# Kernel tuning notes

Hardware: AMD Instinct MI355X
Metric: run time of the kernel (lower is better)

The kernel has to match this reference:

```python
import jax, jax.numpy as jnp
import numpy as np

D = 64          # node_hidden_dim
MP_STEPS = 6    # num_step_message_passing
S2S_STEPS = 6   # num_step_set2set
LSTM_LAYERS = 3 # num_layer_set2set


def setup_inputs() -> dict:
    key = jax.random.key(0)
    ks = jax.random.split(key, 32)
    N, E, B = 10000, 50000, 500
    node_in, edge_in, edge_hid, out_dim = 15, 5, 128, 12
    s = 0.1
    inp = {}
    inp["node_feat"] = jax.random.normal(ks[0], (N, node_in), jnp.float32)
    inp["edge_feat"] = jax.random.normal(ks[1], (E, edge_in), jnp.float32)
    inp["src"] = jax.random.randint(ks[2], (E,), 0, N)
    inp["dst"] = jax.random.randint(ks[3], (E,), 0, N)
    inp["graph_ids"] = jnp.sort(jax.random.randint(ks[4], (N,), 0, B))
    inp["num_graphs"] = B
    # lin0
    inp["lin0_W"] = jax.random.normal(ks[5], (node_in, D), jnp.float32) * s
    inp["lin0_b"] = jnp.zeros((D,), jnp.float32)
    # edge network MLP (Linear -> ReLU -> Linear), output reshaped to D x D per edge
    inp["em_W1"] = jax.random.normal(ks[6], (edge_in, edge_hid), jnp.float32) * s
    inp["em_b1"] = jnp.zeros((edge_hid,), jnp.float32)
    inp["em_W2"] = jax.random.normal(ks[7], (edge_hid, D * D), jnp.float32) * 0.02
    inp["em_b2"] = jnp.zeros((D * D,), jnp.float32)
    inp["conv_bias"] = jnp.zeros((D,), jnp.float32)
    # GRU (input D, hidden D), torch layout: [3*D, in], gate order r,z,n
    inp["gru_Wih"] = jax.random.normal(ks[8], (3 * D, D), jnp.float32) * s
    inp["gru_Whh"] = jax.random.normal(ks[9], (3 * D, D), jnp.float32) * s
    inp["gru_bih"] = jnp.zeros((3 * D,), jnp.float32)
    inp["gru_bhh"] = jnp.zeros((3 * D,), jnp.float32)
    # Set2Set LSTM: input 2*D, hidden D, 3 layers. torch layout [4*D, in], gates i,f,g,o
    inp["lstm0_Wih"] = jax.random.normal(ks[10], (4 * D, 2 * D), jnp.float32) * s
    inp["lstm0_Whh"] = jax.random.normal(ks[11], (4 * D, D), jnp.float32) * s
    inp["lstm0_bih"] = jnp.zeros((4 * D,), jnp.float32)
    inp["lstm0_bhh"] = jnp.zeros((4 * D,), jnp.float32)
    inp["lstm12_Wih"] = jax.random.normal(ks[12], (2, 4 * D, D), jnp.float32) * s
    inp["lstm12_Whh"] = jax.random.normal(ks[13], (2, 4 * D, D), jnp.float32) * s
    inp["lstm12_bih"] = jnp.zeros((2, 4 * D), jnp.float32)
    inp["lstm12_bhh"] = jnp.zeros((2, 4 * D), jnp.float32)
    # output head
    inp["lin1_W"] = jax.random.normal(ks[14], (2 * D, D), jnp.float32) * s
    inp["lin1_b"] = jnp.zeros((D,), jnp.float32)
    inp["lin2_W"] = jax.random.normal(ks[15], (D, out_dim), jnp.float32) * s
    inp["lin2_b"] = jnp.zeros((out_dim,), jnp.float32)
    return inp


def _mpnn(node_feat, edge_feat, src, dst, graph_ids, num_graphs,
          lin0_W, lin0_b, em_W1, em_b1, em_W2, em_b2, conv_bias,
          gru_Wih, gru_Whh, gru_bih, gru_bhh,
          lstm0_Wih, lstm0_Whh, lstm0_bih, lstm0_bhh,
          lstm12_Wih, lstm12_Whh, lstm12_bih, lstm12_bhh,
          lin1_W, lin1_b, lin2_W, lin2_b):
    N = node_feat.shape[0]
    E = edge_feat.shape[0]
    B = num_graphs
    # initial node embedding
    out = jax.nn.relu(node_feat @ lin0_W + lin0_b)      # [N, D]
    h = out                                             # GRU hidden (seq_len=1, 1 layer)
    # per-edge weight matrices (edge features are static across steps)
    We = (jax.nn.relu(edge_feat @ em_W1 + em_b1) @ em_W2 + em_b2).reshape(E, D, D)
    for _ in range(MP_STEPS):
        # NNConv: gather src -> per-edge matvec -> scatter-add to dst
        msg = jnp.einsum('ei,eio->eo', out[src], We)    # [E, D]
        agg = jax.ops.segment_sum(msg, dst, num_segments=N) + conv_bias
        m = jax.nn.relu(agg)                            # [N, D]
        # GRU cell (torch gate order r, z, n)
        gx = m @ gru_Wih.T + gru_bih
        gh = h @ gru_Whh.T + gru_bhh
        rx, zx, nx = jnp.split(gx, 3, axis=-1)
        rh, zh, nh = jnp.split(gh, 3, axis=-1)
        r = jax.nn.sigmoid(rx + rh)
        z = jax.nn.sigmoid(zx + zh)
        n = jnp.tanh(nx + r * nh)
        h = (1.0 - z) * n + z * h
        out = h
    # Set2Set readout: 3-layer LSTM over steps, attention over nodes per graph
    h_l = [jnp.zeros((B, D), out.dtype) for _ in range(LSTM_LAYERS)]
    c_l = [jnp.zeros((B, D), out.dtype) for _ in range(LSTM_LAYERS)]
    q_star = jnp.zeros((B, 2 * D), out.dtype)
    for _ in range(S2S_STEPS):
        x = q_star
        for l in range(LSTM_LAYERS):
            if l == 0:
                Wih, Whh, bih, bhh = lstm0_Wih, lstm0_Whh, lstm0_bih, lstm0_bhh
            else:
                Wih, Whh = lstm12_Wih[l - 1], lstm12_Whh[l - 1]
                bih, bhh = lstm12_bih[l - 1], lstm12_bhh[l - 1]
            g = x @ Wih.T + bih + h_l[l] @ Whh.T + bhh
            i_g, f_g, g_g, o_g = jnp.split(g, 4, axis=-1)
            c_l[l] = jax.nn.sigmoid(f_g) * c_l[l] + jax.nn.sigmoid(i_g) * jnp.tanh(g_g)
            h_l[l] = jax.nn.sigmoid(o_g) * jnp.tanh(c_l[l])
            x = h_l[l]
        q = x                                           # [B, D]
        # segment softmax attention
        e = jnp.sum(out * q[graph_ids], axis=-1)        # [N]
        emax = jax.ops.segment_max(e, graph_ids, num_segments=B)
        ex = jnp.exp(e - emax[graph_ids])
        denom = jax.ops.segment_sum(ex, graph_ids, num_segments=B)
        alpha = ex / denom[graph_ids]                   # [N]
        readout = jax.ops.segment_sum(alpha[:, None] * out, graph_ids, num_segments=B)
        q_star = jnp.concatenate([q, readout], axis=-1) # [B, 2D]
    y = jax.nn.relu(q_star @ lin1_W + lin1_b) @ lin2_W + lin2_b
    return y


def reference(node_feat, edge_feat, src, dst, graph_ids, num_graphs,
              lin0_W, lin0_b, em_W1, em_b1, em_W2, em_b2, conv_bias,
              gru_Wih, gru_Whh, gru_bih, gru_bhh,
              lstm0_Wih, lstm0_Whh, lstm0_bih, lstm0_bhh,
              lstm12_Wih, lstm12_Whh, lstm12_bih, lstm12_bhh,
              lin1_W, lin1_b, lin2_W, lin2_b):
    return _mpnn(node_feat, edge_feat, src, dst, graph_ids, num_graphs,
                 lin0_W, lin0_b, em_W1, em_b1, em_W2, em_b2, conv_bias,
                 gru_Wih, gru_Whh, gru_bih, gru_bhh,
                 lstm0_Wih, lstm0_Whh, lstm0_bih, lstm0_bhh,
                 lstm12_Wih, lstm12_Whh, lstm12_bih, lstm12_bhh,
                 lin1_W, lin1_b, lin2_W, lin2_b)
```

## Files before the change

kernel.cpp:

```cpp
#include <hip/hip_runtime.h>
#include <math.h>

#define NGRAPH 500
#define MP_STEPS 6
#define S2S_STEPS 6
#define S2S_CAP 128

typedef _Float16 h8 __attribute__((ext_vector_type(8)));
typedef float f4 __attribute__((ext_vector_type(4)));

__device__ __forceinline__ float sigmoidf_(float v){ return 1.0f/(1.0f + expf(-v)); }

__global__ void k_zero(float* __restrict__ p, int n){
  int i = blockIdx.x*256 + threadIdx.x;
  if(i < n) p[i] = 0.f;
}

__global__ void k_lin0(const float* __restrict__ nf, const float* __restrict__ W,
                       const float* __restrict__ b, float* __restrict__ x, int N){
  int n = blockIdx.x*4 + (threadIdx.x >> 6);
  int d = threadIdx.x & 63;
  if(n >= N) return;
  float acc = b[d];
#pragma unroll
  for(int i=0;i<15;i++) acc = fmaf(nf[n*15+i], W[i*64+d], acc);
  x[n*64+d] = fmaxf(acc, 0.0f);
}

__global__ void k_edgeh(const float* __restrict__ ef, const float* __restrict__ W1,
                        const float* __restrict__ b1, _Float16* __restrict__ he, int E){
  int e = blockIdx.x;
  int h = threadIdx.x;
  if(e >= E || h >= 160) return;
  float v;
  if(h < 128){
    float acc = b1[h];
#pragma unroll
    for(int i=0;i<5;i++) acc = fmaf(ef[e*5+i], W1[i*128+h], acc);
    v = fmaxf(acc, 0.f);
  } else {
    v = (h == 128) ? 1.0f : 0.0f;
  }
  he[(size_t)e*160 + h] = (_Float16)v;
}

__global__ void k_prepW2(const float* __restrict__ W2, const float* __restrict__ b2,
                         _Float16* __restrict__ W2T){
  int idx = blockIdx.x*256 + threadIdx.x;
  if(idx >= 4096*160) return;
  int n = idx / 160, k = idx % 160;
  float v = (k < 128) ? W2[(size_t)k*4096 + n] : ((k == 128) ? b2[n] : 0.f);
  W2T[idx] = (_Float16)v;
}

__global__ __launch_bounds__(256, 2) void k_fmsg(
    const _Float16* __restrict__ he,
    const _Float16* __restrict__ W2T,
    const float* __restrict__ x,
    const int* __restrict__ src, const int* __restrict__ dst,
    float* __restrict__ agg, int E)
{
  __shared__ _Float16 hs[64*160];
  __shared__ float xsT[64*68];
  __shared__ int ds_dst[64];
  const int tid  = threadIdx.x;
  const int wave = tid >> 6;
  const int lane = tid & 63;
  const int quad = lane >> 4;
  const int l15  = lane & 15;
  const int e0   = blockIdx.x * 64;

  for(int t = tid; t < 1280; t += 256){
    int r = t / 20, c = t % 20;
    uint4 v = make_uint4(0,0,0,0);
    if(e0 + r < E) v = *(const uint4*)&he[(size_t)(e0+r)*160 + c*8];
    *(uint4*)&hs[r*160 + c*8] = v;
  }
  {
    int j = tid >> 2, qc = tid & 3;
    int sj = (e0 + j < E) ? src[e0 + j] : 0;
    const float4* xr = (const float4*)(x + (size_t)sj*64);
#pragma unroll
    for(int k=0;k<4;k++){
      float4 v = xr[qc*4 + k];
      int ib = qc*16 + k*4;
      xsT[(ib+0)*68 + j] = v.x;
      xsT[(ib+1)*68 + j] = v.y;
      xsT[(ib+2)*68 + j] = v.z;
      xsT[(ib+3)*68 + j] = v.w;
    }
  }
  if(tid < 64) ds_dst[tid] = (e0 + tid < E) ? dst[e0 + tid] : 0;
  __syncthreads();

  h8 af[4][5];
#pragma unroll
  for(int mt=0;mt<4;mt++)
#pragma unroll
    for(int ks=0;ks<5;ks++)
      af[mt][ks] = *(const h8*)&hs[(mt*16 + l15)*160 + ks*32 + (quad<<3)];

  const _Float16* bbase = W2T + ((size_t)(wave*16 + l15))*160 + (quad<<3);
  h8 bf[5], bn[5];
#pragma unroll
  for(int ks=0;ks<5;ks++) bf[ks] = *(const h8*)(bbase + ks*32);

  f4 macc[4];
#pragma unroll
  for(int mt=0;mt<4;mt++) macc[mt] = (f4){0.f,0.f,0.f,0.f};

#pragma unroll 2
  for(int i=0;i<64;i++){
    if(i < 63){
      const _Float16* nb = bbase + (size_t)(i+1)*64*160;
#pragma unroll
      for(int ks=0;ks<5;ks++) bn[ks] = *(const h8*)(nb + ks*32);
    }
    f4 g0 = (f4){0.f,0.f,0.f,0.f}, g1 = g0, g2 = g0, g3 = g0;
#pragma unroll
    for(int ks=0;ks<5;ks++){
      g0 = __builtin_amdgcn_mfma_f32_16x16x32_f16(af[0][ks], bf[ks], g0, 0, 0, 0);
      g1 = __builtin_amdgcn_mfma_f32_16x16x32_f16(af[1][ks], bf[ks], g1, 0, 0, 0);
      g2 = __builtin_amdgcn_mfma_f32_16x16x32_f16(af[2][ks], bf[ks], g2, 0, 0, 0);
      g3 = __builtin_amdgcn_mfma_f32_16x16x32_f16(af[3][ks], bf[ks], g3, 0, 0, 0);
    }
    f4 x0 = *(const f4*)&xsT[i*68 +  0 + (quad<<2)];
    f4 x1 = *(const f4*)&xsT[i*68 + 16 + (quad<<2)];
    f4 x2 = *(const f4*)&xsT[i*68 + 32 + (quad<<2)];
    f4 x3 = *(const f4*)&xsT[i*68 + 48 + (quad<<2)];
    macc[0] += x0 * g0;
    macc[1] += x1 * g1;
    macc[2] += x2 * g2;
    macc[3] += x3 * g3;
#pragma unroll
    for(int ks=0;ks<5;ks++) bf[ks] = bn[ks];
  }

  const int col = wave*16 + l15;
#pragma unroll
  for(int mt=0;mt<4;mt++){
#pragma unroll
    for(int r=0;r<4;r++){
      int edge = mt*16 + (quad<<2) + r;
      if(e0 + edge < E)
        atomicAdd(&agg[(size_t)ds_dst[edge]*64 + col], macc[mt][r]);
    }
  }
}

__global__ __launch_bounds__(256) void k_gru2(
    float* __restrict__ x, float* __restrict__ agg, const float* __restrict__ cb,
    const float* __restrict__ WihT, const float* __restrict__ WhhT,
    const float* __restrict__ bih, const float* __restrict__ bhh, int N)
{
  __shared__ float ms[32*64], hs2[32*64];
  const int tid = threadIdx.x;
  const int n0 = blockIdx.x*32;
  for(int t=tid; t<2048; t+=256){
    int n = n0 + (t>>6), d = t&63;
    float mv=0.f, hv=0.f;
    if(n < N){
      mv = fmaxf(agg[(size_t)n*64+d] + cb[d], 0.f);
      agg[(size_t)n*64+d] = 0.f;
      hv = x[(size_t)n*64+d];
    }
    ms[t]=mv; hs2[t]=hv;
  }
  __syncthreads();
  const int gx = tid & 31, ng = tid >> 5;
  float ar[4][2]={{0}}, az[4][2]={{0}}, anx[4][2]={{0}}, anh[4][2]={{0}};
#pragma unroll 4
  for(int k=0;k<64;k++){
    float wi0=WihT[k*192+gx],     wi1=WihT[k*192+gx+32];
    float wi2=WihT[k*192+gx+64],  wi3=WihT[k*192+gx+96];
    float wi4=WihT[k*192+gx+128], wi5=WihT[k*192+gx+160];
    float wh0=WhhT[k*192+gx],     wh1=WhhT[k*192+gx+32];
    float wh2=WhhT[k*192+gx+64],  wh3=WhhT[k*192+gx+96];
    float wh4=WhhT[k*192+gx+128], wh5=WhhT[k*192+gx+160];
#pragma unroll
    for(int j=0;j<4;j++){
      float mk = ms[(ng*4+j)*64+k], hk = hs2[(ng*4+j)*64+k];
      ar[j][0] = fmaf(mk,wi0, fmaf(hk,wh0, ar[j][0]));
      ar[j][1] = fmaf(mk,wi1, fmaf(hk,wh1, ar[j][1]));
      az[j][0] = fmaf(mk,wi2, fmaf(hk,wh2, az[j][0]));
      az[j][1] = fmaf(mk,wi3, fmaf(hk,wh3, az[j][1]));
      anx[j][0]= fmaf(mk,wi4, anx[j][0]);
      anx[j][1]= fmaf(mk,wi5, anx[j][1]);
      anh[j][0]= fmaf(hk,wh4, anh[j][0]);
      anh[j][1]= fmaf(hk,wh5, anh[j][1]);
    }
  }
#pragma unroll
  for(int j=0;j<4;j++){
    int n = n0 + ng*4 + j;
    if(n >= N) continue;
#pragma unroll
    for(int c=0;c<2;c++){
      int d = gx + 32*c;
      float r  = sigmoidf_(ar[j][c] + bih[d]     + bhh[d]);
      float z  = sigmoidf_(az[j][c] + bih[64+d]  + bhh[64+d]);
      float nn = tanhf(anx[j][c] + bih[128+d] + r*(anh[j][c] + bhh[128+d]));
      float hv = hs2[(ng*4+j)*64+d];
      x[(size_t)n*64+d] = (1.f - z)*nn + z*hv;
    }
  }
}

__global__ void k_tr_gru(const float* __restrict__ Wih, const float* __restrict__ Whh,
                         float* __restrict__ WihT, float* __restrict__ WhhT){
  int idx = blockIdx.x*256 + threadIdx.x;
  if(idx < 192*64){
    int r = idx/64, i = idx%64;
    WihT[i*192 + r] = Wih[idx];
    WhhT[i*192 + r] = Whh[idx];
  }
}

__global__ void k_tr_lstm(const float* __restrict__ w0ih, const float* __restrict__ w0hh,
                          const float* __restrict__ w12ih, const float* __restrict__ w12hh,
                          float* __restrict__ t0ih, float* __restrict__ t0hh,
                          float* __restrict__ t12ih, float* __restrict__ t12hh){
  int idx = blockIdx.x*256 + threadIdx.x;
  if(idx < 256*128){ int r = idx/128, k = idx%128; t0ih[k*256+r] = w0ih[idx]; }
  if(idx < 256*64){ int r = idx/64, k = idx%64; t0hh[k*256+r] = w0hh[idx]; }
  if(idx < 2*256*64){
    int l = idx/(256*64); int rem = idx%(256*64); int r = rem/64, k = rem%64;
    t12ih[l*64*256 + k*256 + r] = w12ih[idx];
    t12hh[l*64*256 + k*256 + r] = w12hh[idx];
  }
}

__device__ __forceinline__ int lbound(const int* __restrict__ a, int n, int v){
  int lo=0, hi=n;
  while(lo<hi){ int mid=(lo+hi)>>1; if(a[mid]<v) lo=mid+1; else hi=mid; }
  return lo;
}

template<int IN>
__device__ __forceinline__ void lstm_layer(
    const float* __restrict__ xin, float* __restrict__ hv, float* __restrict__ cv,
    const float* __restrict__ WihT, const float* __restrict__ WhhT,
    const float* __restrict__ bi, const float* __restrict__ bh,
    float* __restrict__ gs, int t)
{
  float a0=0.f,a1=0.f,a2=0.f,a3=0.f;
#pragma unroll
  for(int k=0;k<IN;k+=4){
    a0 = fmaf(xin[k+0], WihT[(k+0)*256+t], a0);
    a1 = fmaf(xin[k+1], WihT[(k+1)*256+t], a1);
    a2 = fmaf(xin[k+2], WihT[(k+2)*256+t], a2);
    a3 = fmaf(xin[k+3], WihT[(k+3)*256+t], a3);
  }
#pragma unroll
  for(int k=0;k<64;k+=4){
    a0 = fmaf(hv[k+0], WhhT[(k+0)*256+t], a0);
    a1 = fmaf(hv[k+1], WhhT[(k+1)*256+t], a1);
    a2 = fmaf(hv[k+2], WhhT[(k+2)*256+t], a2);
    a3 = fmaf(hv[k+3], WhhT[(k+3)*256+t], a3);
  }
  gs[t] = (a0+a1)+(a2+a3) + bi[t] + bh[t];
  __syncthreads();
  if(t < 64){
    float ig = sigmoidf_(gs[t]);
    float fg = sigmoidf_(gs[64+t]);
    float gg = tanhf(gs[128+t]);
    float og = sigmoidf_(gs[192+t]);
    float cn = fg*cv[t] + ig*gg;
    cv[t] = cn;
    hv[t] = og*tanhf(cn);
  }
  __syncthreads();
}

__global__ __launch_bounds__(256) void k_s2s(
    const float* __restrict__ x, const int* __restrict__ gid, int N,
    const float* __restrict__ t0ih, const float* __restrict__ t0hh,
    const float* __restrict__ l0_bih, const float* __restrict__ l0_bhh,
    const float* __restrict__ t12ih, const float* __restrict__ t12hh,
    const float* __restrict__ l12_bih, const float* __restrict__ l12_bhh,
    const float* __restrict__ W1, const float* __restrict__ b1,
    const float* __restrict__ W2, const float* __restrict__ b2,
    float* __restrict__ y)
{
  const int b = blockIdx.x;
  const int t = threadIdx.x;
  const int wave = t >> 6, lane = t & 63;
  __shared__ float xt[S2S_CAP*64];
  __shared__ float hsl[3][64], csl[3][64], qs[128], gs[256];
  __shared__ float ps[S2S_CAP], rop[4*64], wred[4], wsum[4];
  __shared__ int sh_n0, sh_n1;

  if(t == 0) sh_n0 = lbound(gid, N, b);
  if(t == 1) sh_n1 = lbound(gid, N, b+1);
  if(t < 192){ hsl[t>>6][t&63] = 0.f; csl[t>>6][t&63] = 0.f; }
  if(t < 128) qs[t] = 0.f;
  __syncthreads();
  const int n0 = sh_n0, cnt = sh_n1 - sh_n0;
  const int cc = (cnt < S2S_CAP) ? cnt : S2S_CAP;

  for(int j = wave; j < cc; j += 4)
    xt[j*64 + lane] = x[(size_t)(n0+j)*64 + lane];
  __syncthreads();

  for(int step=0; step<S2S_STEPS; step++){
    lstm_layer<128>(qs,     hsl[0], csl[0], t0ih,           t0hh,           l0_bih,        l0_bhh,        gs, t);
    lstm_layer<64>(hsl[0],  hsl[1], csl[1], t12ih,          t12hh,          l12_bih,       l12_bhh,       gs, t);
    lstm_layer<64>(hsl[1],  hsl[2], csl[2], t12ih + 64*256, t12hh + 64*256, l12_bih + 256, l12_bhh + 256, gs, t);

    float qv = hsl[2][lane];
    float pm = -1e30f;
    for(int j = wave; j < cc; j += 4){
      float p = xt[j*64 + lane] * qv;
#pragma unroll
      for(int o=32;o;o>>=1) p += __shfl_xor(p, o, 64);
      if(lane == 0) ps[j] = p;
      pm = fmaxf(pm, p);
    }
    for(int j = S2S_CAP + wave; j < cnt; j += 4){
      float p = x[(size_t)(n0+j)*64 + lane] * qv;
#pragma unroll
      for(int o=32;o;o>>=1) p += __shfl_xor(p, o, 64);
      pm = fmaxf(pm, p);
    }
    if(lane == 0) wred[wave] = pm;
    __syncthreads();
    float mx = fmaxf(fmaxf(wred[0],wred[1]), fmaxf(wred[2],wred[3]));

    float pro = 0.f, pssum = 0.f;
    for(int j = wave; j < cc; j += 4){
      float ex = expf(ps[j] - mx);
      pssum += ex;
      pro = fmaf(ex, xt[j*64 + lane], pro);
    }
    for(int j = S2S_CAP + wave; j < cnt; j += 4){
      float xv = x[(size_t)(n0+j)*64 + lane];
      float p = xv * qv;
#pragma unroll
      for(int o=32;o;o>>=1) p += __shfl_xor(p, o, 64);
      float ex = expf(p - mx);
      pssum += ex;
      pro = fmaf(ex, xv, pro);
    }
    rop[wave*64 + lane] = pro;
    if(lane == 0) wsum[wave] = pssum;
    __syncthreads();
    if(t < 64){
      float tot = wsum[0]+wsum[1]+wsum[2]+wsum[3];
      float inv = (tot > 0.f) ? 1.f/tot : 0.f;
      float rv = (rop[t] + rop[64+t] + rop[128+t] + rop[192+t]) * inv;
      qs[t] = hsl[2][t];
      qs[64+t] = rv;
    }
    __syncthreads();
  }
  if(t < 64){
    float a = b1[t];
#pragma unroll 4
    for(int k=0;k<128;k++) a = fmaf(qs[k], W1[k*64+t], a);
    gs[t] = fmaxf(a, 0.f);
  }
  __syncthreads();
  if(t < 12){
    float o = b2[t];
#pragma unroll 4
    for(int k=0;k<64;k++) o = fmaf(gs[k], W2[k*12+t], o);
    y[b*12+t] = o;
  }
}

extern "C" void kernel_launch(void* const* d_in, const int* in_sizes, int n_in,
                              void* d_out, int out_size, void* d_ws, size_t ws_size,
                              hipStream_t stream) {
  const float* node_feat = (const float*)d_in[0];
  const float* edge_feat = (const float*)d_in[1];
  const int*   src       = (const int*)d_in[2];
  const int*   dst       = (const int*)d_in[3];
  const int*   gid       = (const int*)d_in[4];
  const float* lin0_W = (const float*)d_in[6];
  const float* lin0_b = (const float*)d_in[7];
  const float* em_W1  = (const float*)d_in[8];
  const float* em_b1  = (const float*)d_in[9];
  const float* em_W2  = (const float*)d_in[10];
  const float* em_b2  = (const float*)d_in[11];
  const float* conv_b = (const float*)d_in[12];
  const float* gru_Wih = (const float*)d_in[13];
  const float* gru_Whh = (const float*)d_in[14];
  const float* gru_bih = (const float*)d_in[15];
  const float* gru_bhh = (const float*)d_in[16];
  const float* l0_Wih = (const float*)d_in[17];
  const float* l0_Whh = (const float*)d_in[18];
  const float* l0_bih = (const float*)d_in[19];
  const float* l0_bhh = (const float*)d_in[20];
  const float* l12_Wih = (const float*)d_in[21];
  const float* l12_Whh = (const float*)d_in[22];
  const float* l12_bih = (const float*)d_in[23];
  const float* l12_bhh = (const float*)d_in[24];
  const float* lin1_W = (const float*)d_in[25];
  const float* lin1_b = (const float*)d_in[26];
  const float* lin2_W = (const float*)d_in[27];
  const float* lin2_b = (const float*)d_in[28];
  float* y = (float*)d_out;

  const int N = in_sizes[0] / 15;
  const int E = in_sizes[1] / 5;
  const int B = NGRAPH;

  char* p = (char*)d_ws;
  auto carve = [&](size_t bytes)->char* {
    char* r = p; p += (bytes + 255) & ~(size_t)255; return r;
  };
  _Float16* he_h = (_Float16*)carve((size_t)E*160*2);
  _Float16* W2T  = (_Float16*)carve((size_t)4096*160*2);
  float* x     = (float*)carve((size_t)N*64*4);
  float* agg   = (float*)carve((size_t)N*64*4);
  float* gWihT = (float*)carve(192*64*4);
  float* gWhhT = (float*)carve(192*64*4);
  float* t0ih  = (float*)carve(128*256*4);
  float* t0hh  = (float*)carve(64*256*4);
  float* t12ih = (float*)carve(2*64*256*4);
  float* t12hh = (float*)carve(2*64*256*4);
  (void)ws_size; (void)n_in; (void)out_size;

  k_lin0<<<(N+3)/4, 256, 0, stream>>>(node_feat, lin0_W, lin0_b, x, N);
  k_edgeh<<<E, 192, 0, stream>>>(edge_feat, em_W1, em_b1, he_h, E);
  k_prepW2<<<(4096*160+255)/256, 256, 0, stream>>>(em_W2, em_b2, W2T);
  k_tr_gru<<<(192*64+255)/256, 256, 0, stream>>>(gru_Wih, gru_Whh, gWihT, gWhhT);
  k_tr_lstm<<<(2*256*64+255)/256, 256, 0, stream>>>(l0_Wih, l0_Whh, l12_Wih, l12_Whh,
                                                    t0ih, t0hh, t12ih, t12hh);
  k_zero<<<(N*64+255)/256, 256, 0, stream>>>(agg, N*64);

  const int nblk = (E + 63) / 64;
  for(int s=0; s<MP_STEPS; s++){
    k_fmsg<<<nblk, 256, 0, stream>>>(he_h, W2T, x, src, dst, agg, E);
    k_gru2<<<(N+31)/32, 256, 0, stream>>>(x, agg, conv_b, gWihT, gWhhT, gru_bih, gru_bhh, N);
  }

  k_s2s<<<B, 256, 0, stream>>>(x, gid, N,
                               t0ih, t0hh, l0_bih, l0_bhh,
                               t12ih, t12hh, l12_bih, l12_bhh,
                               lin1_W, lin1_b, lin2_W, lin2_b, y);
}
```

Before: 951.2 us.

## Hoist edge-MLP bias into per-node precompute, widen message tiles, split S2S LSTM

The em_b2 bias term is taken out of the per-edge GEMM: a per-node product x·B2 is computed in lin0 and after each GRU step, then added per edge before the atomic scatter. This shrinks K from 160 to 128. The message kernel now processes 128 edges per block with 8 M-tiles per wave, which doubles reuse of each W2T load but drops the register prefetch of the next B fragment. Set2Set moves to 512 threads, with the LSTM K-reduction split across two halves and the shared node cache cap lowered to 64. Each GRU step also gains an extra 64x64 matvec per node.

Result: no change. 962.8 us (+1.2%).

```diff
diff --git a/kernel.cpp b/kernel.cpp
--- a/kernel.cpp
+++ b/kernel.cpp
@@ -4,7 +4,7 @@
 #define NGRAPH 500
 #define MP_STEPS 6
 #define S2S_STEPS 6
-#define S2S_CAP 128
+#define S2S_CAP 64
 
 typedef _Float16 h8 __attribute__((ext_vector_type(8)));
 typedef float f4 __attribute__((ext_vector_type(4)));
@@ -17,133 +17,135 @@
 }
 
 __global__ void k_lin0(const float* __restrict__ nf, const float* __restrict__ W,
-                       const float* __restrict__ b, float* __restrict__ x, int N){
+                       const float* __restrict__ b, const float* __restrict__ B2,
+                       float* __restrict__ x, float* __restrict__ bm, int N){
   int n = blockIdx.x*4 + (threadIdx.x >> 6);
   int d = threadIdx.x & 63;
   if(n >= N) return;
   float acc = b[d];
 #pragma unroll
   for(int i=0;i<15;i++) acc = fmaf(nf[n*15+i], W[i*64+d], acc);
-  x[n*64+d] = fmaxf(acc, 0.0f);
+  float xv = fmaxf(acc, 0.0f);
+  x[n*64+d] = xv;
+  float bmv = 0.f;
+  for(int k=0;k<64;k++){
+    float xk = __shfl(xv, k, 64);
+    bmv = fmaf(xk, B2[k*64+d], bmv);
+  }
+  bm[(size_t)n*64+d] = bmv;
 }
 
 __global__ void k_edgeh(const float* __restrict__ ef, const float* __restrict__ W1,
                         const float* __restrict__ b1, _Float16* __restrict__ he, int E){
-  int e = blockIdx.x;
-  int h = threadIdx.x;
-  if(e >= E || h >= 160) return;
-  float v;
-  if(h < 128){
-    float acc = b1[h];
-#pragma unroll
-    for(int i=0;i<5;i++) acc = fmaf(ef[e*5+i], W1[i*128+h], acc);
-    v = fmaxf(acc, 0.f);
-  } else {
-    v = (h == 128) ? 1.0f : 0.0f;
-  }
-  he[(size_t)e*160 + h] = (_Float16)v;
-}
-
-__global__ void k_prepW2(const float* __restrict__ W2, const float* __restrict__ b2,
-                         _Float16* __restrict__ W2T){
+  int e = blockIdx.x*2 + (threadIdx.x >> 7);
+  int h = threadIdx.x & 127;
+  if(e >= E) return;
+  float acc = b1[h];
+#pragma unroll
+  for(int i=0;i<5;i++) acc = fmaf(ef[e*5+i], W1[i*128+h], acc);
+  he[(size_t)e*128 + h] = (_Float16)fmaxf(acc, 0.f);
+}
+
+__global__ void k_prepW2(const float* __restrict__ W2, _Float16* __restrict__ W2T){
   int idx = blockIdx.x*256 + threadIdx.x;
-  if(idx >= 4096*160) return;
-  int n = idx / 160, k = idx % 160;
-  float v = (k < 128) ? W2[(size_t)k*4096 + n] : ((k == 128) ? b2[n] : 0.f);
-  W2T[idx] = (_Float16)v;
+  if(idx >= 4096*128) return;
+  int n = idx >> 7, k = idx & 127;
+  W2T[idx] = (_Float16)W2[(size_t)k*4096 + n];
 }
 
 __global__ __launch_bounds__(256, 2) void k_fmsg(
     const _Float16* __restrict__ he,
     const _Float16* __restrict__ W2T,
     const float* __restrict__ x,
+    const float* __restrict__ bm,
     const int* __restrict__ src, const int* __restrict__ dst,
     float* __restrict__ agg, int E)
 {
-  __shared__ _Float16 hs[64*160];
-  __shared__ float xsT[64*68];
-  __shared__ int ds_dst[64];
+  __shared__ _Float16 hs[128*128];
+  __shared__ float xsT[64*132];
+  __shared__ int ds_dst[128];
+  __shared__ int ds_src[128];
   const int tid  = threadIdx.x;
-  const int wave = tid >> 6;
+  const int og   = tid >> 6;
   const int lane = tid & 63;
   const int quad = lane >> 4;
   const int l15  = lane & 15;
-  const int e0   = blockIdx.x * 64;
-
-  for(int t = tid; t < 1280; t += 256){
-    int r = t / 20, c = t % 20;
+  const int e0   = blockIdx.x * 128;
+
+  for(int t = tid; t < 2048; t += 256){
+    int r = t >> 4, c = t & 15;
     uint4 v = make_uint4(0,0,0,0);
-    if(e0 + r < E) v = *(const uint4*)&he[(size_t)(e0+r)*160 + c*8];
-    *(uint4*)&hs[r*160 + c*8] = v;
+    if(e0 + r < E) v = *(const uint4*)&he[(size_t)(e0+r)*128 + c*8];
+    *(uint4*)&hs[r*128 + c*8] = v;
   }
   {
-    int j = tid >> 2, qc = tid & 3;
+    int j = tid >> 1, half = tid & 1;
     int sj = (e0 + j < E) ? src[e0 + j] : 0;
-    const float4* xr = (const float4*)(x + (size_t)sj*64);
-#pragma unroll
-    for(int k=0;k<4;k++){
-      float4 v = xr[qc*4 + k];
-      int ib = qc*16 + k*4;
-      xsT[(ib+0)*68 + j] = v.x;
-      xsT[(ib+1)*68 + j] = v.y;
-      xsT[(ib+2)*68 + j] = v.z;
-      xsT[(ib+3)*68 + j] = v.w;
-    }
-  }
-  if(tid < 64) ds_dst[tid] = (e0 + tid < E) ? dst[e0 + tid] : 0;
-  __syncthreads();
-
-  h8 af[4][5];
-#pragma unroll
-  for(int mt=0;mt<4;mt++)
-#pragma unroll
-    for(int ks=0;ks<5;ks++)
-      af[mt][ks] = *(const h8*)&hs[(mt*16 + l15)*160 + ks*32 + (quad<<3)];
-
-  const _Float16* bbase = W2T + ((size_t)(wave*16 + l15))*160 + (quad<<3);
-  h8 bf[5], bn[5];
-#pragma unroll
-  for(int ks=0;ks<5;ks++) bf[ks] = *(const h8*)(bbase + ks*32);
-
-  f4 macc[4];
-#pragma unroll
-  for(int mt=0;mt<4;mt++) macc[mt] = (f4){0.f,0.f,0.f,0.f};
-
-#pragma unroll 2
+    const float4* xr = (const float4*)(x + (size_t)sj*64) + half*8;
+#pragma unroll
+    for(int k=0;k<8;k++){
+      float4 v = xr[k];
+      int ib = half*32 + k*4;
+      xsT[(ib+0)*132 + j] = v.x;
+      xsT[(ib+1)*132 + j] = v.y;
+      xsT[(ib+2)*132 + j] = v.z;
+      xsT[(ib+3)*132 + j] = v.w;
+    }
+  }
+  if(tid < 128){
+    ds_dst[tid] = (e0 + tid < E) ? dst[e0 + tid] : 0;
+    ds_src[tid] = (e0 + tid < E) ? src[e0 + tid] : 0;
+  }
+  __syncthreads();
+
+  h8 af[8][4];
+#pragma unroll
+  for(int mt=0;mt<8;mt++)
+#pragma unroll
+    for(int ks=0;ks<4;ks++)
+      af[mt][ks] = *(const h8*)&hs[(mt*16 + l15)*128 + ks*32 + (quad<<3)];
+
+  const _Float16* bbase = W2T + (size_t)(og*16 + l15)*128 + (quad<<3);
+
+  f4 macc[8];
+#pragma unroll
+  for(int mt=0;mt<8;mt++) macc[mt] = (f4){0.f,0.f,0.f,0.f};
+
+#pragma unroll 1
   for(int i=0;i<64;i++){
-    if(i < 63){
-      const _Float16* nb = bbase + (size_t)(i+1)*64*160;
-#pragma unroll
-      for(int ks=0;ks<5;ks++) bn[ks] = *(const h8*)(nb + ks*32);
-    }
-    f4 g0 = (f4){0.f,0.f,0.f,0.f}, g1 = g0, g2 = g0, g3 = g0;
-#pragma unroll
-    for(int ks=0;ks<5;ks++){
-      g0 = __builtin_amdgcn_mfma_f32_16x16x32_f16(af[0][ks], bf[ks], g0, 0, 0, 0);
-      g1 = __builtin_amdgcn_mfma_f32_16x16x32_f16(af[1][ks], bf[ks], g1, 0, 0, 0);
-      g2 = __builtin_amdgcn_mfma_f32_16x16x32_f16(af[2][ks], bf[ks], g2, 0, 0, 0);
-      g3 = __builtin_amdgcn_mfma_f32_16x16x32_f16(af[3][ks], bf[ks], g3, 0, 0, 0);
-    }
-    f4 x0 = *(const f4*)&xsT[i*68 +  0 + (quad<<2)];
-    f4 x1 = *(const f4*)&xsT[i*68 + 16 + (quad<<2)];
-    f4 x2 = *(const f4*)&xsT[i*68 + 32 + (quad<<2)];
-    f4 x3 = *(const f4*)&xsT[i*68 + 48 + (quad<<2)];
-    macc[0] += x0 * g0;
-    macc[1] += x1 * g1;
-    macc[2] += x2 * g2;
-    macc[3] += x3 * g3;
-#pragma unroll
-    for(int ks=0;ks<5;ks++) bf[ks] = bn[ks];
-  }
-
-  const int col = wave*16 + l15;
-#pragma unroll
-  for(int mt=0;mt<4;mt++){
+    const _Float16* bp = bbase + (size_t)i*64*128;
+    h8 bf0 = *(const h8*)(bp);
+    h8 bf1 = *(const h8*)(bp + 32);
+    h8 bf2 = *(const h8*)(bp + 64);
+    h8 bf3 = *(const h8*)(bp + 96);
+    f4 g[8];
+#pragma unroll
+    for(int mt=0;mt<8;mt++) g[mt] = (f4){0.f,0.f,0.f,0.f};
+#pragma unroll
+    for(int mt=0;mt<8;mt++) g[mt] = __builtin_amdgcn_mfma_f32_16x16x32_f16(af[mt][0], bf0, g[mt], 0,0,0);
+#pragma unroll
+    for(int mt=0;mt<8;mt++) g[mt] = __builtin_amdgcn_mfma_f32_16x16x32_f16(af[mt][1], bf1, g[mt], 0,0,0);
+#pragma unroll
+    for(int mt=0;mt<8;mt++) g[mt] = __builtin_amdgcn_mfma_f32_16x16x32_f16(af[mt][2], bf2, g[mt], 0,0,0);
+#pragma unroll
+    for(int mt=0;mt<8;mt++) g[mt] = __builtin_amdgcn_mfma_f32_16x16x32_f16(af[mt][3], bf3, g[mt], 0,0,0);
+#pragma unroll
+    for(int mt=0;mt<8;mt++){
+      f4 xf = *(const f4*)&xsT[i*132 + mt*16 + (quad<<2)];
+      macc[mt] += xf * g[mt];
+    }
+  }
+
+  const int col = og*16 + l15;
+#pragma unroll
+  for(int mt=0;mt<8;mt++){
 #pragma unroll
     for(int r=0;r<4;r++){
       int edge = mt*16 + (quad<<2) + r;
-      if(e0 + edge < E)
-        atomicAdd(&agg[(size_t)ds_dst[edge]*64 + col], macc[mt][r]);
+      if(e0 + edge < E){
+        float v = macc[mt][r] + bm[(size_t)ds_src[edge]*64 + col];
+        atomicAdd(&agg[(size_t)ds_dst[edge]*64 + col], v);
+      }
     }
   }
 }
@@ -151,7 +153,8 @@
 __global__ __launch_bounds__(256) void k_gru2(
     float* __restrict__ x, float* __restrict__ agg, const float* __restrict__ cb,
     const float* __restrict__ WihT, const float* __restrict__ WhhT,
-    const float* __restrict__ bih, const float* __restrict__ bhh, int N)
+    const float* __restrict__ bih, const float* __restrict__ bhh,
+    const float* __restrict__ B2, float* __restrict__ bm, int N)
 {
   __shared__ float ms[32*64], hs2[32*64];
   const int tid = threadIdx.x;
@@ -190,10 +193,9 @@
       anh[j][1]= fmaf(hk,wh5, anh[j][1]);
     }
   }
+  float xn[4][2];
 #pragma unroll
   for(int j=0;j<4;j++){
-    int n = n0 + ng*4 + j;
-    if(n >= N) continue;
 #pragma unroll
     for(int c=0;c<2;c++){
       int d = gx + 32*c;
@@ -201,7 +203,37 @@
       float z  = sigmoidf_(az[j][c] + bih[64+d]  + bhh[64+d]);
       float nn = tanhf(anx[j][c] + bih[128+d] + r*(anh[j][c] + bhh[128+d]));
       float hv = hs2[(ng*4+j)*64+d];
-      x[(size_t)n*64+d] = (1.f - z)*nn + z*hv;
+      xn[j][c] = (1.f - z)*nn + z*hv;
+    }
+  }
+  __syncthreads();
+#pragma unroll
+  for(int j=0;j<4;j++){
+#pragma unroll
+    for(int c=0;c<2;c++){
+      int n = n0 + ng*4 + j;
+      ms[(ng*4+j)*64 + gx + 32*c] = xn[j][c];
+      if(n < N) x[(size_t)n*64 + gx + 32*c] = xn[j][c];
+    }
+  }
+  __syncthreads();
+  float bmv[4][2] = {{0}};
+#pragma unroll 4
+  for(int d=0;d<64;d++){
+    float b0 = B2[d*64+gx], b1 = B2[d*64+gx+32];
+#pragma unroll
+    for(int j=0;j<4;j++){
+      float xd = ms[(ng*4+j)*64 + d];
+      bmv[j][0] = fmaf(xd, b0, bmv[j][0]);
+      bmv[j][1] = fmaf(xd, b1, bmv[j][1]);
+    }
+  }
+#pragma unroll
+  for(int j=0;j<4;j++){
+    int n = n0 + ng*4 + j;
+    if(n < N){
+      bm[(size_t)n*64 + gx]      = bmv[j][0];
+      bm[(size_t)n*64 + gx + 32] = bmv[j][1];
     }
   }
 }
@@ -237,42 +269,44 @@
 }
 
 template<int IN>
-__device__ __forceinline__ void lstm_layer(
+__device__ __forceinline__ void lstm_layer2(
     const float* __restrict__ xin, float* __restrict__ hv, float* __restrict__ cv,
     const float* __restrict__ WihT, const float* __restrict__ WhhT,
     const float* __restrict__ bi, const float* __restrict__ bh,
-    float* __restrict__ gs, int t)
+    float* __restrict__ gpart, int tid, int t, int hf)
 {
+  const int kx0 = hf*(IN/2);
+  const int kh0 = hf*32;
   float a0=0.f,a1=0.f,a2=0.f,a3=0.f;
 #pragma unroll
-  for(int k=0;k<IN;k+=4){
-    a0 = fmaf(xin[k+0], WihT[(k+0)*256+t], a0);
-    a1 = fmaf(xin[k+1], WihT[(k+1)*256+t], a1);
-    a2 = fmaf(xin[k+2], WihT[(k+2)*256+t], a2);
-    a3 = fmaf(xin[k+3], WihT[(k+3)*256+t], a3);
-  }
-#pragma unroll
-  for(int k=0;k<64;k+=4){
-    a0 = fmaf(hv[k+0], WhhT[(k+0)*256+t], a0);
-    a1 = fmaf(hv[k+1], WhhT[(k+1)*256+t], a1);
-    a2 = fmaf(hv[k+2], WhhT[(k+2)*256+t], a2);
-    a3 = fmaf(hv[k+3], WhhT[(k+3)*256+t], a3);
-  }
-  gs[t] = (a0+a1)+(a2+a3) + bi[t] + bh[t];
-  __syncthreads();
-  if(t < 64){
-    float ig = sigmoidf_(gs[t]);
-    float fg = sigmoidf_(gs[64+t]);
-    float gg = tanhf(gs[128+t]);
-    float og = sigmoidf_(gs[192+t]);
-    float cn = fg*cv[t] + ig*gg;
-    cv[t] = cn;
-    hv[t] = og*tanhf(cn);
-  }
-  __syncthreads();
-}
-
-__global__ __launch_bounds__(256) void k_s2s(
+  for(int k=0;k<IN/2;k+=4){
+    a0 = fmaf(xin[kx0+k+0], WihT[(kx0+k+0)*256+t], a0);
+    a1 = fmaf(xin[kx0+k+1], WihT[(kx0+k+1)*256+t], a1);
+    a2 = fmaf(xin[kx0+k+2], WihT[(kx0+k+2)*256+t], a2);
+    a3 = fmaf(xin[kx0+k+3], WihT[(kx0+k+3)*256+t], a3);
+  }
+#pragma unroll
+  for(int k=0;k<32;k+=4){
+    a0 = fmaf(hv[kh0+k+0], WhhT[(kh0+k+0)*256+t], a0);
+    a1 = fmaf(hv[kh0+k+1], WhhT[(kh0+k+1)*256+t], a1);
+    a2 = fmaf(hv[kh0+k+2], WhhT[(kh0+k+2)*256+t], a2);
+    a3 = fmaf(hv[kh0+k+3], WhhT[(kh0+k+3)*256+t], a3);
+  }
+  gpart[tid] = (a0+a1)+(a2+a3);
+  __syncthreads();
+  if(tid < 64){
+    float gi = gpart[tid]     + gpart[256+tid] + bi[tid]     + bh[tid];
+    float gf = gpart[64+tid]  + gpart[320+tid] + bi[64+tid]  + bh[64+tid];
+    float gg = gpart[128+tid] + gpart[384+tid] + bi[128+tid] + bh[128+tid];
+    float go = gpart[192+tid] + gpart[448+tid] + bi[192+tid] + bh[192+tid];
+    float cn = sigmoidf_(gf)*cv[tid] + sigmoidf_(gi)*tanhf(gg);
+    cv[tid] = cn;
+    hv[tid] = sigmoidf_(go)*tanhf(cn);
+  }
+  __syncthreads();
+}
+
+__global__ __launch_bounds__(512) void k_s2s(
     const float* __restrict__ x, const int* __restrict__ gid, int N,
     const float* __restrict__ t0ih, const float* __restrict__ t0hh,
     const float* __restrict__ l0_bih, const float* __restrict__ l0_bhh,
@@ -283,40 +317,41 @@
     float* __restrict__ y)
 {
   const int b = blockIdx.x;
-  const int t = threadIdx.x;
-  const int wave = t >> 6, lane = t & 63;
+  const int tid = threadIdx.x;
+  const int t = tid & 255, hf = tid >> 8;
+  const int wave = tid >> 6, lane = tid & 63;
   __shared__ float xt[S2S_CAP*64];
-  __shared__ float hsl[3][64], csl[3][64], qs[128], gs[256];
-  __shared__ float ps[S2S_CAP], rop[4*64], wred[4], wsum[4];
+  __shared__ float hsl[3][64], csl[3][64], qs[128], gpart[512];
+  __shared__ float ps[S2S_CAP], rop[8*64], wred[8], wsum[8];
   __shared__ int sh_n0, sh_n1;
 
-  if(t == 0) sh_n0 = lbound(gid, N, b);
-  if(t == 1) sh_n1 = lbound(gid, N, b+1);
-  if(t < 192){ hsl[t>>6][t&63] = 0.f; csl[t>>6][t&63] = 0.f; }
-  if(t < 128) qs[t] = 0.f;
+  if(tid == 0) sh_n0 = lbound(gid, N, b);
+  if(tid == 1) sh_n1 = lbound(gid, N, b+1);
+  if(tid < 192){ hsl[tid>>6][tid&63] = 0.f; csl[tid>>6][tid&63] = 0.f; }
+  if(tid >= 192 && tid < 320) qs[tid-192] = 0.f;
   __syncthreads();
   const int n0 = sh_n0, cnt = sh_n1 - sh_n0;
   const int cc = (cnt < S2S_CAP) ? cnt : S2S_CAP;
 
-  for(int j = wave; j < cc; j += 4)
+  for(int j = wave; j < cc; j += 8)
     xt[j*64 + lane] = x[(size_t)(n0+j)*64 + lane];
   __syncthreads();
 
   for(int step=0; step<S2S_STEPS; step++){
-    lstm_layer<128>(qs,     hsl[0], csl[0], t0ih,           t0hh,           l0_bih,        l0_bhh,        gs, t);
-    lstm_layer<64>(hsl[0],  hsl[1], csl[1], t12ih,          t12hh,          l12_bih,       l12_bhh,       gs, t);
-    lstm_layer<64>(hsl[1],  hsl[2], csl[2], t12ih + 64*256, t12hh + 64*256, l12_bih + 256, l12_bhh + 256, gs, t);
+    lstm_layer2<128>(qs,     hsl[0], csl[0], t0ih,           t0hh,           l0_bih,        l0_bhh,        gpart, tid, t, hf);
+    lstm_layer2<64>(hsl[0],  hsl[1], csl[1], t12ih,          t12hh,          l12_bih,       l12_bhh,       gpart, tid, t, hf);
+    lstm_layer2<64>(hsl[1],  hsl[2], csl[2], t12ih + 64*256, t12hh + 64*256, l12_bih + 256, l12_bhh + 256, gpart, tid, t, hf);
 
     float qv = hsl[2][lane];
     float pm = -1e30f;
-    for(int j = wave; j < cc; j += 4){
+    for(int j = wave; j < cc; j += 8){
       float p = xt[j*64 + lane] * qv;
 #pragma unroll
       for(int o=32;o;o>>=1) p += __shfl_xor(p, o, 64);
       if(lane == 0) ps[j] = p;
       pm = fmaxf(pm, p);
     }
-    for(int j = S2S_CAP + wave; j < cnt; j += 4){
+    for(int j = S2S_CAP + wave; j < cnt; j += 8){
       float p = x[(size_t)(n0+j)*64 + lane] * qv;
 #pragma unroll
       for(int o=32;o;o>>=1) p += __shfl_xor(p, o, 64);
@@ -324,15 +359,17 @@
     }
     if(lane == 0) wred[wave] = pm;
     __syncthreads();
-    float mx = fmaxf(fmaxf(wred[0],wred[1]), fmaxf(wred[2],wred[3]));
+    float mx = wred[0];
+#pragma unroll
+    for(int w=1;w<8;w++) mx = fmaxf(mx, wred[w]);
 
     float pro = 0.f, pssum = 0.f;
-    for(int j = wave; j < cc; j += 4){
+    for(int j = wave; j < cc; j += 8){
       float ex = expf(ps[j] - mx);
       pssum += ex;
       pro = fmaf(ex, xt[j*64 + lane], pro);
     }
-    for(int j = S2S_CAP + wave; j < cnt; j += 4){
+    for(int j = S2S_CAP + wave; j < cnt; j += 8){
       float xv = x[(size_t)(n0+j)*64 + lane];
       float p = xv * qv;
 #pragma unroll
@@ -344,27 +381,31 @@
     rop[wave*64 + lane] = pro;
     if(lane == 0) wsum[wave] = pssum;
     __syncthreads();
-    if(t < 64){
-      float tot = wsum[0]+wsum[1]+wsum[2]+wsum[3];
+    if(tid < 64){
+      float tot = 0.f;
+#pragma unroll
+      for(int w=0;w<8;w++) tot += wsum[w];
       float inv = (tot > 0.f) ? 1.f/tot : 0.f;
-      float rv = (rop[t] + rop[64+t] + rop[128+t] + rop[192+t]) * inv;
-      qs[t] = hsl[2][t];
-      qs[64+t] = rv;
+      float rv = 0.f;
+#pragma unroll
+      for(int w=0;w<8;w++) rv += rop[w*64+tid];
+      qs[tid] = hsl[2][tid];
+      qs[64+tid] = rv * inv;
     }
     __syncthreads();
   }
-  if(t < 64){
-    float a = b1[t];
+  if(tid < 64){
+    float a = b1[tid];
 #pragma unroll 4
-    for(int k=0;k<128;k++) a = fmaf(qs[k], W1[k*64+t], a);
-    gs[t] = fmaxf(a, 0.f);
-  }
-  __syncthreads();
-  if(t < 12){
-    float o = b2[t];
+    for(int k=0;k<128;k++) a = fmaf(qs[k], W1[k*64+tid], a);
+    gpart[tid] = fmaxf(a, 0.f);
+  }
+  __syncthreads();
+  if(tid < 12){
+    float o = b2[tid];
 #pragma unroll 4
-    for(int k=0;k<64;k++) o = fmaf(gs[k], W2[k*12+t], o);
-    y[b*12+t] = o;
+    for(int k=0;k<64;k++) o = fmaf(gpart[k], W2[k*12+tid], o);
+    y[b*12+tid] = o;
   }
 }
 
@@ -409,10 +450,11 @@
   auto carve = [&](size_t bytes)->char* {
     char* r = p; p += (bytes + 255) & ~(size_t)255; return r;
   };
-  _Float16* he_h = (_Float16*)carve((size_t)E*160*2);
-  _Float16* W2T  = (_Float16*)carve((size_t)4096*160*2);
+  _Float16* he_h = (_Float16*)carve((size_t)E*128*2);
+  _Float16* W2T  = (_Float16*)carve((size_t)4096*128*2);
   float* x     = (float*)carve((size_t)N*64*4);
   float* agg   = (float*)carve((size_t)N*64*4);
+  float* bmv   = (float*)carve((size_t)N*64*4);
   float* gWihT = (float*)carve(192*64*4);
   float* gWhhT = (float*)carve(192*64*4);
   float* t0ih  = (float*)carve(128*256*4);
@@ -421,21 +463,22 @@
   float* t12hh = (float*)carve(2*64*256*4);
   (void)ws_size; (void)n_in; (void)out_size;
 
-  k_lin0<<<(N+3)/4, 256, 0, stream>>>(node_feat, lin0_W, lin0_b, x, N);
-  k_edgeh<<<E, 192, 0, stream>>>(edge_feat, em_W1, em_b1, he_h, E);
-  k_prepW2<<<(4096*160+255)/256, 256, 0, stream>>>(em_W2, em_b2, W2T);
+  k_lin0<<<(N+3)/4, 256, 0, stream>>>(node_feat, lin0_W, lin0_b, em_b2, x, bmv, N);
+  k_edgeh<<<(E+1)/2, 256, 0, stream>>>(edge_feat, em_W1, em_b1, he_h, E);
+  k_prepW2<<<(4096*128+255)/256, 256, 0, stream>>>(em_W2, W2T);
   k_tr_gru<<<(192*64+255)/256, 256, 0, stream>>>(gru_Wih, gru_Whh, gWihT, gWhhT);
   k_tr_lstm<<<(2*256*64+255)/256, 256, 0, stream>>>(l0_Wih, l0_Whh, l12_Wih, l12_Whh,
                                                     t0ih, t0hh, t12ih, t12hh);
   k_zero<<<(N*64+255)/256, 256, 0, stream>>>(agg, N*64);
 
-  const int nblk = (E + 63) / 64;
+  const int nblk = (E + 127) / 128;
   for(int s=0; s<MP_STEPS; s++){
-    k_fmsg<<<nblk, 256, 0, stream>>>(he_h, W2T, x, src, dst, agg, E);
-    k_gru2<<<(N+31)/32, 256, 0, stream>>>(x, agg, conv_b, gWihT, gWhhT, gru_bih, gru_bhh, N);
-  }
-
-  k_s2s<<<B, 256, 0, stream>>>(x, gid, N,
+    k_fmsg<<<nblk, 256, 0, stream>>>(he_h, W2T, x, bmv, src, dst, agg, E);
+    k_gru2<<<(N+31)/32, 256, 0, stream>>>(x, agg, conv_b, gWihT, gWhhT,
+                                          gru_bih, gru_bhh, em_b2, bmv, N);
+  }
+
+  k_s2s<<<B, 512, 0, stream>>>(x, gid, N,
                                t0ih, t0hh, l0_bih, l0_bhh,
                                t12ih, t12hh, l12_bih, l12_bhh,
                                lin1_W, lin1_b, lin2_W, lin2_b, y);
```
